# Kernel optimization log

Measured on AMD Instinct MI355X. Metric: run time of the kernel, lower is better.

Reference implementation:

```python
import jax, jax.numpy as jnp
import numpy as np

H = 4
N = 1024
E = 4096
LE = 16384
FN = 128
FE = 64
FNO = 128
FEO = 64


def _lin(x, W, b):
    # torch nn.Linear: y = x @ W.T + b, W is [out, in]
    return x @ W.T + b


def setup_inputs() -> dict:
    key = jax.random.key(0)
    ks = jax.random.split(key, 24)
    s = 0.05
    inp = {}
    inp["node_inputs"] = jax.random.normal(ks[0], (N, FN), jnp.float32)
    inp["edge_inputs"] = jax.random.normal(ks[1], (E, FE), jnp.float32)
    inp["src"] = jax.random.randint(ks[2], (E,), 0, N, jnp.int32)
    inp["dst"] = jax.random.randint(ks[3], (E,), 0, N, jnp.int32)
    inp["lg_src"] = jax.random.randint(ks[4], (LE,), 0, E, jnp.int32)
    inp["lg_dst"] = jax.random.randint(ks[5], (LE,), 0, E, jnp.int32)
    # projection linear weights (torch Linear layout [out, in])
    inp["nqW"] = jax.random.normal(ks[6], (H * FN, FN), jnp.float32) * s
    inp["nqb"] = jax.random.normal(ks[7], (H * FN,), jnp.float32) * s
    inp["nkW"] = jax.random.normal(ks[8], (H, FN), jnp.float32) * s
    inp["nkb"] = jax.random.normal(ks[9], (H,), jnp.float32) * s
    inp["nvW"] = jax.random.normal(ks[10], (H * FN, FN), jnp.float32) * s
    inp["nvb"] = jax.random.normal(ks[11], (H * FN,), jnp.float32) * s
    inp["eqW"] = jax.random.normal(ks[12], (H * FE, FE), jnp.float32) * s
    inp["eqb"] = jax.random.normal(ks[13], (H * FE,), jnp.float32) * s
    inp["ekW"] = jax.random.normal(ks[14], (H, FE), jnp.float32) * s
    inp["ekb"] = jax.random.normal(ks[15], (H,), jnp.float32) * s
    inp["evW"] = jax.random.normal(ks[16], (H * FE, FE), jnp.float32) * s
    inp["evb"] = jax.random.normal(ks[17], (H * FE,), jnp.float32) * s
    # convolution output linears
    inp["ncW"] = jax.random.normal(ks[18], (FNO, FN), jnp.float32) * s
    inp["ncb"] = jax.random.normal(ks[19], (FNO,), jnp.float32) * s
    inp["ecW"] = jax.random.normal(ks[20], (FEO, FE), jnp.float32) * s
    inp["ecb"] = jax.random.normal(ks[21], (FEO,), jnp.float32) * s
    return inp


def reference(node_inputs, edge_inputs, src, dst, lg_src, lg_dst,
              nqW, nqb, nkW, nkb, nvW, nvb,
              eqW, eqb, ekW, ekb, evW, evb,
              ncW, ncb, ecW, ecb):
    n, fn = node_inputs.shape
    e, fe = edge_inputs.shape
    # per-head Q/K/V projections; .view(H, -1, F) == row-major reshape
    nq = _lin(node_inputs, nqW, nqb).reshape(H, -1, fn)   # [H,N,FN]
    nk = _lin(node_inputs, nkW, nkb).reshape(H, -1, 1)    # [H,N,1]
    nv = _lin(node_inputs, nvW, nvb).reshape(H, -1, fn)   # [H,N,FN]
    eq = _lin(edge_inputs, eqW, eqb).reshape(H, -1, fe)   # [H,E,FE]
    ek = _lin(edge_inputs, ekW, ekb).reshape(H, -1, 1)    # [H,E,1]
    ev = _lin(edge_inputs, evW, evb).reshape(H, -1, fe)   # [H,E,FE]
    # self attention: softmax(Q @ Q^T @ K, dim=1); associate as Q @ (Q^T K)
    node_sa = jax.nn.softmax(nq @ (jnp.swapaxes(nq, -1, -2) @ nk), axis=1)  # [H,N,1]
    edge_sa = jax.nn.softmax(eq @ (jnp.swapaxes(eq, -1, -2) @ ek), axis=1)  # [H,E,1]
    # vectorized edge-indexed scatter of attention scores into dense projections
    node_proj = jnp.zeros((H, n, n), node_inputs.dtype).at[:, src, dst].set(edge_sa[:, :, 0])
    conn = dst[lg_src]  # g.find_edges(source)[1]: destination node of edge lg_src
    edge_proj = jnp.zeros((H, e, e), edge_inputs.dtype).at[:, lg_src, lg_dst].set(node_sa[:, conn, 0])
    # dense adjacency matrices
    A = jnp.zeros((n, n), node_inputs.dtype).at[src, dst].set(1.0)
    Alg = jnp.zeros((e, e), edge_inputs.dtype).at[lg_src, lg_dst].set(1.0)
    # 'sum' aggregation: (attn_proj * A) @ value, then Linear + relu
    node_out = jax.nn.relu(_lin((node_proj * A) @ nv, ncW, ncb))   # [H,N,FNO]
    edge_out = jax.nn.relu(_lin((edge_proj * Alg) @ ev, ecW, ecb)) # [H,E,FEO]
    return (node_out, edge_out)
```

## Files before the change

### kernel.cpp

```cpp
#include <hip/hip_runtime.h>

#define H_ 4
#define N_ 1024
#define E_ 4096
#define LE_ 16384
#define FN_ 128
#define FE_ 64
#define CAP_ 32

struct P {
  const float *Xn, *Xe;
  const int *src, *dst, *lgs, *lgd;
  const float *nqW, *nqb, *nkW, *nkb, *nvW, *nvb;
  const float *eqW, *eqb, *ekW, *ekb, *evW, *evb;
  const float *ncW, *ncb, *ecW, *ecb;
  float *out;
  float *NV, *EV, *nsa, *esa;
};

template<int K, bool RELU>
__device__ void gemm_tile(const float* __restrict__ X, const float* __restrict__ W,
                          const float* __restrict__ b, float* __restrict__ C,
                          int O, int r0, int o0, float* smem, int t) {
  float* Xs = smem;
  float* Ws = smem + 2048;
  const int tn = t & 15, tm = t >> 4;
  float acc[4][4] = {};
  for (int k0 = 0; k0 < K; k0 += 32) {
#pragma unroll
    for (int ph = 0; ph < 2; ++ph) {
      int i4 = t + ph * 256;
      int m = i4 >> 3;
      int k4 = (i4 & 7) << 2;
      int m4 = m >> 2, ml = m & 3;
      float4 vx = *(const float4*)&X[(r0 + m) * K + k0 + k4];
      float4 vw = *(const float4*)&W[(o0 + m) * K + k0 + k4];
      Xs[(k4 + 0) * 64 + ((m4 ^ ((k4 + 0) & 15)) << 2) + ml] = vx.x;
      Xs[(k4 + 1) * 64 + ((m4 ^ ((k4 + 1) & 15)) << 2) + ml] = vx.y;
      Xs[(k4 + 2) * 64 + ((m4 ^ ((k4 + 2) & 15)) << 2) + ml] = vx.z;
      Xs[(k4 + 3) * 64 + ((m4 ^ ((k4 + 3) & 15)) << 2) + ml] = vx.w;
      Ws[(k4 + 0) * 64 + ((m4 ^ ((k4 + 0) & 15)) << 2) + ml] = vw.x;
      Ws[(k4 + 1) * 64 + ((m4 ^ ((k4 + 1) & 15)) << 2) + ml] = vw.y;
      Ws[(k4 + 2) * 64 + ((m4 ^ ((k4 + 2) & 15)) << 2) + ml] = vw.z;
      Ws[(k4 + 3) * 64 + ((m4 ^ ((k4 + 3) & 15)) << 2) + ml] = vw.w;
    }
    __syncthreads();
#pragma unroll
    for (int k = 0; k < 32; ++k) {
      float4 a = *(const float4*)&Xs[k * 64 + ((tm ^ (k & 15)) << 2)];
      float4 b4 = *(const float4*)&Ws[k * 64 + ((tn ^ (k & 15)) << 2)];
      acc[0][0] += a.x * b4.x; acc[0][1] += a.x * b4.y; acc[0][2] += a.x * b4.z; acc[0][3] += a.x * b4.w;
      acc[1][0] += a.y * b4.x; acc[1][1] += a.y * b4.y; acc[1][2] += a.y * b4.z; acc[1][3] += a.y * b4.w;
      acc[2][0] += a.z * b4.x; acc[2][1] += a.z * b4.y; acc[2][2] += a.z * b4.z; acc[2][3] += a.z * b4.w;
      acc[3][0] += a.w * b4.x; acc[3][1] += a.w * b4.y; acc[3][2] += a.w * b4.z; acc[3][3] += a.w * b4.w;
    }
    __syncthreads();
  }
  float4 bv = *(const float4*)&b[o0 + tn * 4];
#pragma unroll
  for (int i = 0; i < 4; ++i) {
    float4 o;
    o.x = acc[i][0] + bv.x; o.y = acc[i][1] + bv.y;
    o.z = acc[i][2] + bv.z; o.w = acc[i][3] + bv.w;
    if (RELU) {
      o.x = fmaxf(o.x, 0.f); o.y = fmaxf(o.y, 0.f);
      o.z = fmaxf(o.z, 0.f); o.w = fmaxf(o.w, 0.f);
    }
    *(float4*)&C[(r0 + tm * 4 + i) * O + o0 + tn * 4] = o;
  }
}

__global__ __launch_bounds__(1024) void kA(P p) {
  __shared__ float smem[16384];
  const int tid = threadIdx.x;
  const int bid = blockIdx.x;

  if (bid >= 8) {
    if (tid < 512) {
      const int gg = (bid - 8) * 2 + (tid >> 8);
      const int ts_ = tid & 255;
      float* gsm = smem + (tid >> 8) * 4096;
      if (gg % 3 == 0) {
        const int tile = gg / 3;
        gemm_tile<128, false>(p.Xn, p.nvW, p.nvb, p.NV, 512,
                              (tile >> 3) * 64, (tile & 7) * 64, gsm, ts_);
      } else {
        const int tile = gg - gg / 3 - 1;
        gemm_tile<64, false>(p.Xe, p.evW, p.evb, p.EV, 256,
                             (tile >> 2) * 64, (tile & 3) * 64, gsm, ts_);
        __syncthreads(); __syncthreads(); __syncthreads(); __syncthreads();
      }
    } else {
#pragma unroll
      for (int q = 0; q < 8; ++q) __syncthreads();
    }
    return;
  }

  float4* accs = (float4*)smem;
  float* red = smem + 4096;
  float* ys  = smem + 5120;
  float* ts  = smem + 5632;
  float* zs  = smem + 5760;
  float* ds  = smem + 6288;
  float* sig = smem + 6292;
  float* Ks  = smem + 6304;

  if (bid < 4) {
    const int h = bid;
    const int r0 = h * 256;
    float* wkw = Ks + 1024;
    for (int i = tid; i < 512; i += 1024) wkw[i] = p.nkW[i];
    __syncthreads();
    {
      const int rl = tid >> 2, c = tid & 3;
      const float4* x4 = (const float4*)(p.Xn + (r0 + rl) * FN_);
      const float4* w4 = (const float4*)(wkw + c * FN_);
      float acc = p.nkb[c];
      for (int k = 0; k < 32; ++k) {
        float4 x = x4[k], w = w4[k];
        acc += x.x * w.x + x.y * w.y + x.z * w.z + x.w * w.w;
      }
      Ks[tid] = acc;
    }
    __syncthreads();
    {
      int g = tid & 127, q = tid >> 7;
      const float4* Ks4 = (const float4*)Ks;
      float a0 = 0, a1 = 0, a2 = 0, a3 = 0;
      for (int jj = 0; jj < 32; ++jj) {
        int lr = q * 32 + jj;
        float x = p.Xn[(r0 + lr) * FN_ + g];
        float4 k = Ks4[lr];
        a0 += x * k.x; a1 += x * k.y; a2 += x * k.z; a3 += x * k.w;
      }
      accs[tid] = make_float4(a0, a1, a2, a3);
    }
    __syncthreads();
    for (int off = 512; off >= 128; off >>= 1) {
      if (tid < off) {
        float4 a = accs[tid], b = accs[tid + off];
        accs[tid] = make_float4(a.x + b.x, a.y + b.y, a.z + b.z, a.w + b.w);
      }
      __syncthreads();
    }
    if (tid < 128) {
      float4 a = accs[tid];
      ys[tid * 4 + 0] = a.x; ys[tid * 4 + 1] = a.y;
      ys[tid * 4 + 2] = a.z; ys[tid * 4 + 3] = a.w;
    }
    if (tid >= 128 && tid < 160) {
      int t2 = tid - 128, c = t2 & 3, part = t2 >> 2;
      float s = 0.f;
      for (int j = 0; j < 32; ++j) s += Ks[(part * 32 + j) * 4 + c];
      red[t2] = s;
    }
    __syncthreads();
    if (tid < 4) { float s = 0.f; for (int q = 0; q < 8; ++q) s += red[q * 4 + tid]; sig[tid] = s; }
    __syncthreads();
    if (tid < 512) {
      const float4* w4 = (const float4*)(p.nqW + tid * FN_);
      int c = tid >> 7;
      float s = 0.f;
      for (int g4 = 0; g4 < 32; ++g4) {
        float4 w = w4[g4];
        s += w.x * ys[(g4 * 4 + 0) * 4 + c] + w.y * ys[(g4 * 4 + 1) * 4 + c]
           + w.z * ys[(g4 * 4 + 2) * 4 + c] + w.w * ys[(g4 * 4 + 3) * 4 + c];
      }
      red[tid] = s;
    }
    __syncthreads();
    if (tid < 128) {
      float s = red[tid] + red[128 + tid] + red[256 + tid] + red[384 + tid];
      float bb = 0.f;
      for (int c = 0; c < 4; ++c) bb += p.nqb[c * 128 + tid] * sig[c];
      ts[tid] = s + bb;
    }
    __syncthreads();
    if (tid < 512) {
      int c = tid >> 7, g = tid & 127;
      float s = 0.f;
      for (int f = 0; f < 128; ++f) s += p.nqW[(c * 128 + f) * 128 + g] * ts[f];
      zs[c * 132 + g] = s;
    }
    if (tid >= 512 && tid < 516) {
      int c = tid - 512;
      float s = 0.f;
      for (int f = 0; f < 128; ++f) s += p.nqb[c * 128 + f] * ts[f];
      ds[c] = s;
    }
    __syncthreads();
    float sc;
    {
      int c = tid & 3, j = tid >> 2;
      const float4* x4 = (const float4*)(p.Xn + (r0 + j) * FN_);
      const float* z = zs + c * 132;
      float s = ds[c];
      for (int g4 = 0; g4 < 32; ++g4) {
        float4 x = x4[g4];
        s += x.x * z[g4 * 4] + x.y * z[g4 * 4 + 1] + x.z * z[g4 * 4 + 2] + x.w * z[g4 * 4 + 3];
      }
      sc = s;
    }
    red[tid] = sc;
    __syncthreads();
    for (int off = 512; off > 0; off >>= 1) {
      if (tid < off) red[tid] = fmaxf(red[tid], red[tid + off]);
      __syncthreads();
    }
    float m = red[0];
    __syncthreads();
    float e = expf(sc - m);
    red[tid] = e;
    __syncthreads();
    for (int off = 512; off > 0; off >>= 1) {
      if (tid < off) red[tid] += red[tid + off];
      __syncthreads();
    }
    p.nsa[h * N_ + tid] = e / red[0];
  } else {
    const int h = bid - 4;
    const int r0 = h * 1024;
    float* wkw = Ks + 4096;
    for (int i = tid; i < 256; i += 1024) wkw[i] = p.ekW[i];
    __syncthreads();
    {
      const float4* x4 = (const float4*)(p.Xe + (r0 + tid) * FE_);
      const float4* w0 = (const float4*)wkw;
      const float4* w1 = (const float4*)(wkw + 64);
      const float4* w2 = (const float4*)(wkw + 128);
      const float4* w3 = (const float4*)(wkw + 192);
      float a0 = p.ekb[0], a1 = p.ekb[1], a2 = p.ekb[2], a3 = p.ekb[3];
      for (int k = 0; k < 16; ++k) {
        float4 x = x4[k];
        float4 u0 = w0[k], u1 = w1[k], u2 = w2[k], u3 = w3[k];
        a0 += x.x * u0.x + x.y * u0.y + x.z * u0.z + x.w * u0.w;
        a1 += x.x * u1.x + x.y * u1.y + x.z * u1.z + x.w * u1.w;
        a2 += x.x * u2.x + x.y * u2.y + x.z * u2.z + x.w * u2.w;
        a3 += x.x * u3.x + x.y * u3.y + x.z * u3.z + x.w * u3.w;
      }
      Ks[tid * 4 + 0] = a0; Ks[tid * 4 + 1] = a1;
      Ks[tid * 4 + 2] = a2; Ks[tid * 4 + 3] = a3;
    }
    __syncthreads();
    {
      int g = tid & 63, q = tid >> 6;
      const float4* Ks4 = (const float4*)Ks;
      float a0 = 0, a1 = 0, a2 = 0, a3 = 0;
      for (int jj = 0; jj < 64; ++jj) {
        int lr = q * 64 + jj;
        float x = p.Xe[(r0 + lr) * FE_ + g];
        float4 k = Ks4[lr];
        a0 += x * k.x; a1 += x * k.y; a2 += x * k.z; a3 += x * k.w;
      }
      accs[tid] = make_float4(a0, a1, a2, a3);
    }
    __syncthreads();
    for (int off = 512; off >= 64; off >>= 1) {
      if (tid < off) {
        float4 a = accs[tid], b = accs[tid + off];
        accs[tid] = make_float4(a.x + b.x, a.y + b.y, a.z + b.z, a.w + b.w);
      }
      __syncthreads();
    }
    if (tid < 64) {
      float4 a = accs[tid];
      ys[tid * 4 + 0] = a.x; ys[tid * 4 + 1] = a.y;
      ys[tid * 4 + 2] = a.z; ys[tid * 4 + 3] = a.w;
    }
    if (tid >= 128 && tid < 160) {
      int t2 = tid - 128, c = t2 & 3, part = t2 >> 2;
      float s = 0.f;
      for (int j = 0; j < 128; ++j) s += Ks[(part * 128 + j) * 4 + c];
      red[t2] = s;
    }
    __syncthreads();
    if (tid < 4) { float s = 0.f; for (int q = 0; q < 8; ++q) s += red[q * 4 + tid]; sig[tid] = s; }
    __syncthreads();
    if (tid < 256) {
      const float4* w4 = (const float4*)(p.eqW + tid * FE_);
      int c = tid >> 6;
      float s = 0.f;
      for (int g4 = 0; g4 < 16; ++g4) {
        float4 w = w4[g4];
        s += w.x * ys[(g4 * 4 + 0) * 4 + c] + w.y * ys[(g4 * 4 + 1) * 4 + c]
           + w.z * ys[(g4 * 4 + 2) * 4 + c] + w.w * ys[(g4 * 4 + 3) * 4 + c];
      }
      red[tid] = s;
    }
    __syncthreads();
    if (tid < 64) {
      float s = red[tid] + red[64 + tid] + red[128 + tid] + red[192 + tid];
      float bb = 0.f;
      for (int c = 0; c < 4; ++c) bb += p.eqb[c * 64 + tid] * sig[c];
      ts[tid] = s + bb;
    }
    __syncthreads();
    if (tid < 256) {
      int c = tid >> 6, g = tid & 63;
      float s = 0.f;
      for (int f = 0; f < 64; ++f) s += p.eqW[(c * 64 + f) * 64 + g] * ts[f];
      zs[c * 132 + g] = s;
    }
    if (tid >= 256 && tid < 260) {
      int c = tid - 256;
      float s = 0.f;
      for (int f = 0; f < 64; ++f) s += p.eqb[c * 64 + f] * ts[f];
      ds[c] = s;
    }
    __syncthreads();
    float s4[4];
    {
      const float4* x4 = (const float4*)(p.Xe + (r0 + tid) * FE_);
      s4[0] = ds[0]; s4[1] = ds[1]; s4[2] = ds[2]; s4[3] = ds[3];
      for (int g4 = 0; g4 < 16; ++g4) {
        float4 x = x4[g4];
#pragma unroll
        for (int c = 0; c < 4; ++c) {
          const float* z = zs + c * 132 + g4 * 4;
          s4[c] += x.x * z[0] + x.y * z[1] + x.z * z[2] + x.w * z[3];
        }
      }
    }
    float lm = fmaxf(fmaxf(s4[0], s4[1]), fmaxf(s4[2], s4[3]));
    red[tid] = lm;
    __syncthreads();
    for (int off = 512; off > 0; off >>= 1) {
      if (tid < off) red[tid] = fmaxf(red[tid], red[tid + off]);
      __syncthreads();
    }
    float m = red[0];
    __syncthreads();
    float e0 = expf(s4[0] - m), e1 = expf(s4[1] - m);
    float e2 = expf(s4[2] - m), e3 = expf(s4[3] - m);
    red[tid] = e0 + e1 + e2 + e3;
    __syncthreads();
    for (int off = 512; off > 0; off >>= 1) {
      if (tid < off) red[tid] += red[tid + off];
      __syncthreads();
    }
    float inv = 1.f / red[0];
    ((float4*)(p.esa + h * E_))[tid] = make_float4(e0 * inv, e1 * inv, e2 * inv, e3 * inv);
  }
}

__global__ __launch_bounds__(256) void kC(P p) {
  __shared__ float smem[10240];
  __shared__ int cnt_s[64];
  __shared__ int list_s[64 * CAP_];
  const int t = threadIdx.x, bid = blockIdx.x;
  float* Xs = smem;
  float* Ws = smem + 8192;
  const int tn = t & 15, tm = t >> 4;

  if (bid < 128) {
    const int rt = bid >> 1, o0 = (bid & 1) << 6;
    const int h = rt >> 4, p0 = (rt & 15) << 6;
    if (t < 64) cnt_s[t] = 0;
    __syncthreads();
    {
      const int4* src4 = (const int4*)p.src;
      const int4* dst4 = (const int4*)p.dst;
      for (int i4 = t; i4 < E_ / 4; i4 += 256) {
        int4 sv = src4[i4], dv = dst4[i4];
        int sa[4] = {sv.x, sv.y, sv.z, sv.w};
        int da[4] = {dv.x, dv.y, dv.z, dv.w};
#pragma unroll
        for (int j = 0; j < 4; ++j) {
          int ls = sa[j] - p0;
          if ((unsigned)ls < 64u) {
            int pos = atomicAdd(&cnt_s[ls], 1) & (CAP_ - 1);
            list_s[ls * CAP_ + pos] = (da[j] << 12) | (i4 * 4 + j);
          }
        }
      }
    }
    __syncthreads();
    {
      const int m = t >> 2, q = t & 3;
      const int deg = min(cnt_s[m], CAP_);
      const int* lst = list_s + m * CAP_;
      float4 acc[8];
#pragma unroll
      for (int f = 0; f < 8; ++f) acc[f] = make_float4(0.f, 0.f, 0.f, 0.f);
      const float4* NV4 = (const float4*)p.NV + (h << 15);
      const float* esah = p.esa + h * E_;
      for (int i = 0; i < deg; ++i) {
        int pk = lst[i];
        bool win = true;
        for (int i2 = 0; i2 < deg; ++i2) {
          int pk2 = lst[i2];
          if ((pk2 >> 12) == (pk >> 12) && pk2 > pk) win = false;
        }
        if (!win) continue;
        int e = pk & (E_ - 1), d = pk >> 12;
        float a = esah[e];
        const float4* v4 = NV4 + (d << 5);
#pragma unroll
        for (int f = 0; f < 8; ++f) {
          float4 v = v4[q + (f << 2)];
          acc[f].x += a * v.x; acc[f].y += a * v.y;
          acc[f].z += a * v.z; acc[f].w += a * v.w;
        }
      }
      const int m4 = m >> 2, ml = m & 3;
#pragma unroll
      for (int f = 0; f < 8; ++f) {
        int k4 = (q + (f << 2)) << 2;
        Xs[(k4 + 0) * 64 + ((m4 ^ ((k4 + 0) & 15)) << 2) + ml] = acc[f].x;
        Xs[(k4 + 1) * 64 + ((m4 ^ ((k4 + 1) & 15)) << 2) + ml] = acc[f].y;
        Xs[(k4 + 2) * 64 + ((m4 ^ ((k4 + 2) & 15)) << 2) + ml] = acc[f].z;
        Xs[(k4 + 3) * 64 + ((m4 ^ ((k4 + 3) & 15)) << 2) + ml] = acc[f].w;
      }
    }
    float c16[4][4] = {};
    for (int k0 = 0; k0 < 128; k0 += 32) {
#pragma unroll
      for (int ph = 0; ph < 2; ++ph) {
        int i4 = t + ph * 256;
        int mw = i4 >> 3, k4 = (i4 & 7) << 2;
        int w4i = mw >> 2, wl = mw & 3;
        float4 vw = *(const float4*)&p.ncW[(o0 + mw) * 128 + k0 + k4];
        Ws[(k4 + 0) * 64 + ((w4i ^ ((k4 + 0) & 15)) << 2) + wl] = vw.x;
        Ws[(k4 + 1) * 64 + ((w4i ^ ((k4 + 1) & 15)) << 2) + wl] = vw.y;
        Ws[(k4 + 2) * 64 + ((w4i ^ ((k4 + 2) & 15)) << 2) + wl] = vw.z;
        Ws[(k4 + 3) * 64 + ((w4i ^ ((k4 + 3) & 15)) << 2) + wl] = vw.w;
      }
      __syncthreads();
#pragma unroll
      for (int kk = 0; kk < 32; ++kk) {
        int k = k0 + kk;
        float4 a = *(const float4*)&Xs[k * 64 + ((tm ^ (k & 15)) << 2)];
        float4 b4 = *(const float4*)&Ws[kk * 64 + ((tn ^ (kk & 15)) << 2)];
        c16[0][0] += a.x * b4.x; c16[0][1] += a.x * b4.y; c16[0][2] += a.x * b4.z; c16[0][3] += a.x * b4.w;
        c16[1][0] += a.y * b4.x; c16[1][1] += a.y * b4.y; c16[1][2] += a.y * b4.z; c16[1][3] += a.y * b4.w;
        c16[2][0] += a.z * b4.x; c16[2][1] += a.z * b4.y; c16[2][2] += a.z * b4.z; c16[2][3] += a.z * b4.w;
        c16[3][0] += a.w * b4.x; c16[3][1] += a.w * b4.y; c16[3][2] += a.w * b4.z; c16[3][3] += a.w * b4.w;
      }
      __syncthreads();
    }
    float4 bv = *(const float4*)&p.ncb[o0 + tn * 4];
#pragma unroll
    for (int i = 0; i < 4; ++i) {
      float4 o;
      o.x = fmaxf(c16[i][0] + bv.x, 0.f); o.y = fmaxf(c16[i][1] + bv.y, 0.f);
      o.z = fmaxf(c16[i][2] + bv.z, 0.f); o.w = fmaxf(c16[i][3] + bv.w, 0.f);
      *(float4*)&p.out[((h << 10) + p0 + tm * 4 + i) * 128 + o0 + tn * 4] = o;
    }
  } else {
    const int rt = bid - 128;
    const int h = rt >> 6, j0 = (rt & 63) << 6;
    if (t < 64) cnt_s[t] = 0;
    __syncthreads();
    {
      const int4* lgs4 = (const int4*)p.lgs;
      for (int i4 = t; i4 < LE_ / 4; i4 += 256) {
        int4 sv = lgs4[i4];
        int sa[4] = {sv.x, sv.y, sv.z, sv.w};
#pragma unroll
        for (int j = 0; j < 4; ++j) {
          int lj = sa[j] - j0;
          if ((unsigned)lj < 64u) {
            int pos = atomicAdd(&cnt_s[lj], 1) & (CAP_ - 1);
            list_s[lj * CAP_ + pos] = p.lgd[i4 * 4 + j];
          }
        }
      }
    }
    __syncthreads();
    {
      const int m = t >> 2, q = t & 3;
      const int deg = min(cnt_s[m], CAP_);
      const int* lst = list_s + m * CAP_;
      float4 acc[4];
#pragma unroll
      for (int f = 0; f < 4; ++f) acc[f] = make_float4(0.f, 0.f, 0.f, 0.f);
      const float4* EV4 = (const float4*)p.EV + (h << 16);
      for (int i = 0; i < deg; ++i) {
        int c = lst[i];
        bool first = true;
        for (int i2 = 0; i2 < i; ++i2)
          if (lst[i2] == c) first = false;
        if (!first) continue;
        const float4* v4 = EV4 + (c << 4);
#pragma unroll
        for (int f = 0; f < 4; ++f) {
          float4 v = v4[q + (f << 2)];
          acc[f].x += v.x; acc[f].y += v.y; acc[f].z += v.z; acc[f].w += v.w;
        }
      }
      float a = p.nsa[h * N_ + p.dst[j0 + m]];
      const int m4 = m >> 2, ml = m & 3;
#pragma unroll
      for (int f = 0; f < 4; ++f) {
        int k4 = (q + (f << 2)) << 2;
        Xs[(k4 + 0) * 64 + ((m4 ^ ((k4 + 0) & 15)) << 2) + ml] = a * acc[f].x;
        Xs[(k4 + 1) * 64 + ((m4 ^ ((k4 + 1) & 15)) << 2) + ml] = a * acc[f].y;
        Xs[(k4 + 2) * 64 + ((m4 ^ ((k4 + 2) & 15)) << 2) + ml] = a * acc[f].z;
        Xs[(k4 + 3) * 64 + ((m4 ^ ((k4 + 3) & 15)) << 2) + ml] = a * acc[f].w;
      }
    }
    float c16[4][4] = {};
    for (int k0 = 0; k0 < 64; k0 += 32) {
#pragma unroll
      for (int ph = 0; ph < 2; ++ph) {
        int i4 = t + ph * 256;
        int mw = i4 >> 3, k4 = (i4 & 7) << 2;
        int w4i = mw >> 2, wl = mw & 3;
        float4 vw = *(const float4*)&p.ecW[mw * 64 + k0 + k4];
        Ws[(k4 + 0) * 64 + ((w4i ^ ((k4 + 0) & 15)) << 2) + wl] = vw.x;
        Ws[(k4 + 1) * 64 + ((w4i ^ ((k4 + 1) & 15)) << 2) + wl] = vw.y;
        Ws[(k4 + 2) * 64 + ((w4i ^ ((k4 + 2) & 15)) << 2) + wl] = vw.z;
        Ws[(k4 + 3) * 64 + ((w4i ^ ((k4 + 3) & 15)) << 2) + wl] = vw.w;
      }
      __syncthreads();
#pragma unroll
      for (int kk = 0; kk < 32; ++kk) {
        int k = k0 + kk;
        float4 a = *(const float4*)&Xs[k * 64 + ((tm ^ (k & 15)) << 2)];
        float4 b4 = *(const float4*)&Ws[kk * 64 + ((tn ^ (kk & 15)) << 2)];
        c16[0][0] += a.x * b4.x; c16[0][1] += a.x * b4.y; c16[0][2] += a.x * b4.z; c16[0][3] += a.x * b4.w;
        c16[1][0] += a.y * b4.x; c16[1][1] += a.y * b4.y; c16[1][2] += a.y * b4.z; c16[1][3] += a.y * b4.w;
        c16[2][0] += a.z * b4.x; c16[2][1] += a.z * b4.y; c16[2][2] += a.z * b4.z; c16[2][3] += a.z * b4.w;
        c16[3][0] += a.w * b4.x; c16[3][1] += a.w * b4.y; c16[3][2] += a.w * b4.z; c16[3][3] += a.w * b4.w;
      }
      __syncthreads();
    }
    float4 bv = *(const float4*)&p.ecb[tn * 4];
    float* out2 = p.out + 524288;
#pragma unroll
    for (int i = 0; i < 4; ++i) {
      float4 o;
      o.x = fmaxf(c16[i][0] + bv.x, 0.f); o.y = fmaxf(c16[i][1] + bv.y, 0.f);
      o.z = fmaxf(c16[i][2] + bv.z, 0.f); o.w = fmaxf(c16[i][3] + bv.w, 0.f);
      *(float4*)&out2[((h << 12) + j0 + tm * 4 + i) * 64 + tn * 4] = o;
    }
  }
}

extern "C" void kernel_launch(void* const* d_in, const int* in_sizes, int n_in,
                              void* d_out, int out_size, void* d_ws, size_t ws_size,
                              hipStream_t stream) {
  P p;
  p.Xn  = (const float*)d_in[0];
  p.Xe  = (const float*)d_in[1];
  p.src = (const int*)d_in[2];
  p.dst = (const int*)d_in[3];
  p.lgs = (const int*)d_in[4];
  p.lgd = (const int*)d_in[5];
  p.nqW = (const float*)d_in[6];  p.nqb = (const float*)d_in[7];
  p.nkW = (const float*)d_in[8];  p.nkb = (const float*)d_in[9];
  p.nvW = (const float*)d_in[10]; p.nvb = (const float*)d_in[11];
  p.eqW = (const float*)d_in[12]; p.eqb = (const float*)d_in[13];
  p.ekW = (const float*)d_in[14]; p.ekb = (const float*)d_in[15];
  p.evW = (const float*)d_in[16]; p.evb = (const float*)d_in[17];
  p.ncW = (const float*)d_in[18]; p.ncb = (const float*)d_in[19];
  p.ecW = (const float*)d_in[20]; p.ecb = (const float*)d_in[21];
  p.out = (float*)d_out;

  float* f = (float*)d_ws;
  p.NV   = f; f += N_ * H_ * FN_;
  p.EV   = f; f += E_ * H_ * FE_;
  p.nsa  = f; f += H_ * N_;
  p.esa  = f; f += H_ * E_;

  kA<<<200, 1024, 0, stream>>>(p);
  kC<<<384, 256, 0, stream>>>(p);
}
```

Baseline: 152.3 us.

## Use wave-shuffle softmax reductions and double edge tile rows per block

The softmax max/sum reductions in the attention kernel become 64-lane wave shuffles plus a 16-entry shared-memory combine, replacing the 10-step tree that needed a barrier per step. The edge-output part of the second kernel now handles 128 line-graph rows per block instead of 64. That halves the number of times each block scans the full 16K lg_src array and halves the edge block count (256 blocks launched instead of 384). In exchange each thread gathers and accumulates twice as many values, so register use and per-thread work rise, and the grid has fewer blocks to fill the GPU.

Measured after the change: 155.9 us. 2.3% more time.

```diff
diff --git a/kernel.cpp b/kernel.cpp
--- a/kernel.cpp
+++ b/kernel.cpp
@@ -105,6 +105,7 @@
   float* ds  = smem + 6288;
   float* sig = smem + 6292;
   float* Ks  = smem + 6304;
+  const int lane = tid & 63, wid = tid >> 6;
 
   if (bid < 4) {
     const int h = bid;
@@ -202,22 +203,24 @@
       }
       sc = s;
     }
-    red[tid] = sc;
-    __syncthreads();
-    for (int off = 512; off > 0; off >>= 1) {
-      if (tid < off) red[tid] = fmaxf(red[tid], red[tid + off]);
-      __syncthreads();
-    }
-    float m = red[0];
-    __syncthreads();
-    float e = expf(sc - m);
-    red[tid] = e;
-    __syncthreads();
-    for (int off = 512; off > 0; off >>= 1) {
-      if (tid < off) red[tid] += red[tid + off];
-      __syncthreads();
-    }
-    p.nsa[h * N_ + tid] = e / red[0];
+    float mv = sc;
+#pragma unroll
+    for (int off = 32; off; off >>= 1) mv = fmaxf(mv, __shfl_xor(mv, off));
+    if (lane == 0) red[wid] = mv;
+    __syncthreads();
+    float mm = red[0];
+#pragma unroll
+    for (int w = 1; w < 16; ++w) mm = fmaxf(mm, red[w]);
+    float e = expf(sc - mm);
+    float sv = e;
+#pragma unroll
+    for (int off = 32; off; off >>= 1) sv += __shfl_xor(sv, off);
+    if (lane == 0) red[16 + wid] = sv;
+    __syncthreads();
+    float ssum = 0.f;
+#pragma unroll
+    for (int w = 0; w < 16; ++w) ssum += red[16 + w];
+    p.nsa[h * N_ + tid] = e / ssum;
   } else {
     const int h = bid - 4;
     const int r0 = h * 1024;
@@ -322,38 +325,39 @@
         }
       }
     }
-    float lm = fmaxf(fmaxf(s4[0], s4[1]), fmaxf(s4[2], s4[3]));
-    red[tid] = lm;
-    __syncthreads();
-    for (int off = 512; off > 0; off >>= 1) {
-      if (tid < off) red[tid] = fmaxf(red[tid], red[tid + off]);
-      __syncthreads();
-    }
-    float m = red[0];
-    __syncthreads();
-    float e0 = expf(s4[0] - m), e1 = expf(s4[1] - m);
-    float e2 = expf(s4[2] - m), e3 = expf(s4[3] - m);
-    red[tid] = e0 + e1 + e2 + e3;
-    __syncthreads();
-    for (int off = 512; off > 0; off >>= 1) {
-      if (tid < off) red[tid] += red[tid + off];
-      __syncthreads();
-    }
-    float inv = 1.f / red[0];
+    float mv = fmaxf(fmaxf(s4[0], s4[1]), fmaxf(s4[2], s4[3]));
+#pragma unroll
+    for (int off = 32; off; off >>= 1) mv = fmaxf(mv, __shfl_xor(mv, off));
+    if (lane == 0) red[wid] = mv;
+    __syncthreads();
+    float mm = red[0];
+#pragma unroll
+    for (int w = 1; w < 16; ++w) mm = fmaxf(mm, red[w]);
+    float e0 = expf(s4[0] - mm), e1 = expf(s4[1] - mm);
+    float e2 = expf(s4[2] - mm), e3 = expf(s4[3] - mm);
+    float sv = e0 + e1 + e2 + e3;
+#pragma unroll
+    for (int off = 32; off; off >>= 1) sv += __shfl_xor(sv, off);
+    if (lane == 0) red[16 + wid] = sv;
+    __syncthreads();
+    float ssum = 0.f;
+#pragma unroll
+    for (int w = 0; w < 16; ++w) ssum += red[16 + w];
+    float inv = 1.f / ssum;
     ((float4*)(p.esa + h * E_))[tid] = make_float4(e0 * inv, e1 * inv, e2 * inv, e3 * inv);
   }
 }
 
 __global__ __launch_bounds__(256) void kC(P p) {
   __shared__ float smem[10240];
-  __shared__ int cnt_s[64];
-  __shared__ int list_s[64 * CAP_];
+  __shared__ int cnt_s[128];
+  __shared__ int list_s[128 * CAP_];
   const int t = threadIdx.x, bid = blockIdx.x;
   float* Xs = smem;
   float* Ws = smem + 8192;
-  const int tn = t & 15, tm = t >> 4;
 
   if (bid < 128) {
+    const int tn = t & 15, tm = t >> 4;
     const int rt = bid >> 1, o0 = (bid & 1) << 6;
     const int h = rt >> 4, p0 = (rt & 15) << 6;
     if (t < 64) cnt_s[t] = 0;
@@ -449,8 +453,8 @@
     }
   } else {
     const int rt = bid - 128;
-    const int h = rt >> 6, j0 = (rt & 63) << 6;
-    if (t < 64) cnt_s[t] = 0;
+    const int h = rt >> 5, j0 = (rt & 31) << 7;
+    if (t < 128) cnt_s[t] = 0;
     __syncthreads();
     {
       const int4* lgs4 = (const int4*)p.lgs;
@@ -460,7 +464,7 @@
 #pragma unroll
         for (int j = 0; j < 4; ++j) {
           int lj = sa[j] - j0;
-          if ((unsigned)lj < 64u) {
+          if ((unsigned)lj < 128u) {
             int pos = atomicAdd(&cnt_s[lj], 1) & (CAP_ - 1);
             list_s[lj * CAP_ + pos] = p.lgd[i4 * 4 + j];
           }
@@ -469,12 +473,12 @@
     }
     __syncthreads();
     {
-      const int m = t >> 2, q = t & 3;
+      const int m = t >> 1, q = t & 1;
       const int deg = min(cnt_s[m], CAP_);
       const int* lst = list_s + m * CAP_;
-      float4 acc[4];
-#pragma unroll
-      for (int f = 0; f < 4; ++f) acc[f] = make_float4(0.f, 0.f, 0.f, 0.f);
+      float4 acc[8];
+#pragma unroll
+      for (int f = 0; f < 8; ++f) acc[f] = make_float4(0.f, 0.f, 0.f, 0.f);
       const float4* EV4 = (const float4*)p.EV + (h << 16);
       for (int i = 0; i < deg; ++i) {
         int c = lst[i];
@@ -484,23 +488,24 @@
         if (!first) continue;
         const float4* v4 = EV4 + (c << 4);
 #pragma unroll
-        for (int f = 0; f < 4; ++f) {
-          float4 v = v4[q + (f << 2)];
+        for (int f = 0; f < 8; ++f) {
+          float4 v = v4[q + (f << 1)];
           acc[f].x += v.x; acc[f].y += v.y; acc[f].z += v.z; acc[f].w += v.w;
         }
       }
       float a = p.nsa[h * N_ + p.dst[j0 + m]];
       const int m4 = m >> 2, ml = m & 3;
 #pragma unroll
-      for (int f = 0; f < 4; ++f) {
-        int k4 = (q + (f << 2)) << 2;
-        Xs[(k4 + 0) * 64 + ((m4 ^ ((k4 + 0) & 15)) << 2) + ml] = a * acc[f].x;
-        Xs[(k4 + 1) * 64 + ((m4 ^ ((k4 + 1) & 15)) << 2) + ml] = a * acc[f].y;
-        Xs[(k4 + 2) * 64 + ((m4 ^ ((k4 + 2) & 15)) << 2) + ml] = a * acc[f].z;
-        Xs[(k4 + 3) * 64 + ((m4 ^ ((k4 + 3) & 15)) << 2) + ml] = a * acc[f].w;
-      }
-    }
-    float c16[4][4] = {};
+      for (int f = 0; f < 8; ++f) {
+        int k4 = (q + (f << 1)) << 2;
+        Xs[(k4 + 0) * 128 + ((m4 ^ ((k4 + 0) & 31)) << 2) + ml] = a * acc[f].x;
+        Xs[(k4 + 1) * 128 + ((m4 ^ ((k4 + 1) & 31)) << 2) + ml] = a * acc[f].y;
+        Xs[(k4 + 2) * 128 + ((m4 ^ ((k4 + 2) & 31)) << 2) + ml] = a * acc[f].z;
+        Xs[(k4 + 3) * 128 + ((m4 ^ ((k4 + 3) & 31)) << 2) + ml] = a * acc[f].w;
+      }
+    }
+    const int tn = t & 15, tm = t >> 4;
+    float c32[8][4] = {};
     for (int k0 = 0; k0 < 64; k0 += 32) {
 #pragma unroll
       for (int ph = 0; ph < 2; ++ph) {
@@ -517,23 +522,28 @@
 #pragma unroll
       for (int kk = 0; kk < 32; ++kk) {
         int k = k0 + kk;
-        float4 a = *(const float4*)&Xs[k * 64 + ((tm ^ (k & 15)) << 2)];
+        float4 a0 = *(const float4*)&Xs[k * 128 + (((tm * 2) ^ (k & 31)) << 2)];
+        float4 a1 = *(const float4*)&Xs[k * 128 + (((tm * 2 + 1) ^ (k & 31)) << 2)];
         float4 b4 = *(const float4*)&Ws[kk * 64 + ((tn ^ (kk & 15)) << 2)];
-        c16[0][0] += a.x * b4.x; c16[0][1] += a.x * b4.y; c16[0][2] += a.x * b4.z; c16[0][3] += a.x * b4.w;
-        c16[1][0] += a.y * b4.x; c16[1][1] += a.y * b4.y; c16[1][2] += a.y * b4.z; c16[1][3] += a.y * b4.w;
-        c16[2][0] += a.z * b4.x; c16[2][1] += a.z * b4.y; c16[2][2] += a.z * b4.z; c16[2][3] += a.z * b4.w;
-        c16[3][0] += a.w * b4.x; c16[3][1] += a.w * b4.y; c16[3][2] += a.w * b4.z; c16[3][3] += a.w * b4.w;
+        c32[0][0] += a0.x * b4.x; c32[0][1] += a0.x * b4.y; c32[0][2] += a0.x * b4.z; c32[0][3] += a0.x * b4.w;
+        c32[1][0] += a0.y * b4.x; c32[1][1] += a0.y * b4.y; c32[1][2] += a0.y * b4.z; c32[1][3] += a0.y * b4.w;
+        c32[2][0] += a0.z * b4.x; c32[2][1] += a0.z * b4.y; c32[2][2] += a0.z * b4.z; c32[2][3] += a0.z * b4.w;
+        c32[3][0] += a0.w * b4.x; c32[3][1] += a0.w * b4.y; c32[3][2] += a0.w * b4.z; c32[3][3] += a0.w * b4.w;
+        c32[4][0] += a1.x * b4.x; c32[4][1] += a1.x * b4.y; c32[4][2] += a1.x * b4.z; c32[4][3] += a1.x * b4.w;
+        c32[5][0] += a1.y * b4.x; c32[5][1] += a1.y * b4.y; c32[5][2] += a1.y * b4.z; c32[5][3] += a1.y * b4.w;
+        c32[6][0] += a1.z * b4.x; c32[6][1] += a1.z * b4.y; c32[6][2] += a1.z * b4.z; c32[6][3] += a1.z * b4.w;
+        c32[7][0] += a1.w * b4.x; c32[7][1] += a1.w * b4.y; c32[7][2] += a1.w * b4.z; c32[7][3] += a1.w * b4.w;
       }
       __syncthreads();
     }
     float4 bv = *(const float4*)&p.ecb[tn * 4];
     float* out2 = p.out + 524288;
 #pragma unroll
-    for (int i = 0; i < 4; ++i) {
+    for (int i = 0; i < 8; ++i) {
       float4 o;
-      o.x = fmaxf(c16[i][0] + bv.x, 0.f); o.y = fmaxf(c16[i][1] + bv.y, 0.f);
-      o.z = fmaxf(c16[i][2] + bv.z, 0.f); o.w = fmaxf(c16[i][3] + bv.w, 0.f);
-      *(float4*)&out2[((h << 12) + j0 + tm * 4 + i) * 64 + tn * 4] = o;
+      o.x = fmaxf(c32[i][0] + bv.x, 0.f); o.y = fmaxf(c32[i][1] + bv.y, 0.f);
+      o.z = fmaxf(c32[i][2] + bv.z, 0.f); o.w = fmaxf(c32[i][3] + bv.w, 0.f);
+      *(float4*)&out2[((h << 12) + j0 + tm * 8 + i) * 64 + tn * 4] = o;
     }
   }
 }
@@ -565,5 +575,5 @@
   p.esa  = f; f += H_ * E_;
 
   kA<<<200, 1024, 0, stream>>>(p);
-  kC<<<384, 256, 0, stream>>>(p);
+  kC<<<256, 256, 0, stream>>>(p);
 }
```
